# Kernel optimization log

Hardware: AMD Instinct MI355X
Metric: run time of the kernel (lower is better)

## Reference

```python
import jax, jax.numpy as jnp
import numpy as np

B, T, N, D, E = 16, 12, 512, 128, 32  # batch, time, nodes, model_dim, node_emb_dim


def setup_inputs() -> dict:
    key = jax.random.key(0)
    ks = jax.random.split(key, 7)
    return {
        "value": jax.random.normal(ks[0], (B, T, N, D), dtype=jnp.float32),
        "emb": jax.random.normal(ks[1], (T, N, E), dtype=jnp.float32),
        "attn_mask": jax.random.randint(ks[2], (B, N, N), 0, 2, dtype=jnp.int32),
        "W_qk": jax.random.normal(ks[3], (E, D), dtype=jnp.float32) * (1.0 / np.sqrt(E)),
        "b_qk": jax.random.normal(ks[4], (D,), dtype=jnp.float32) * 0.02,
        "W_v": jax.random.normal(ks[5], (D, D), dtype=jnp.float32) * (1.0 / np.sqrt(D)),
        "b_v": jax.random.normal(ks[6], (D,), dtype=jnp.float32) * 0.02,
    }


def reference(value, emb, attn_mask, W_qk, b_qk, W_v, b_v):
    # qk projection shared between query and key: [T, N, D]
    qk = emb @ W_qk + b_qk
    # query: softmax over feature dim D
    q = jax.nn.softmax(qk, axis=-1)                      # [T, N, D]
    # key: transpose then softmax over node dim N
    k = jax.nn.softmax(jnp.swapaxes(qk, -1, -2), axis=-1)  # [T, D, N]
    # value projection (note: out_proj in __init__ is unused in forward)
    v = value @ W_v + b_v                                # [B, T, N, D]
    # batch-independent base attention score, then broadcast over batch
    score = jnp.einsum('tnd,tdm->tnm', q, k)             # [T, N, N]
    score = jnp.broadcast_to(score[None], (value.shape[0],) + score.shape)  # [B, T, N, N]
    # masked fill: mask [B, N, N] -> [B, 1, N, N]
    score = jnp.where(attn_mask[:, None] == 0, jnp.float32(-1e9), score)
    out = jnp.einsum('btnm,btmd->btnd', score, v)         # [B, T, N, D]
    return out
```

## Files before the change

kernel.cpp:

```cpp
#include <hip/hip_runtime.h>

#define B_ 16
#define T_ 12
#define N_ 512
#define D_ 128
#define E_ 32

typedef __attribute__((ext_vector_type(8))) unsigned short u16x8;
typedef __attribute__((ext_vector_type(8))) __bf16 bf16x8;
typedef __attribute__((ext_vector_type(4))) float f32x4;

static __device__ __forceinline__ unsigned short f2bf(float f) {
    unsigned u = __float_as_uint(f);
    unsigned r = (u + 0x7fffu + ((u >> 16) & 1u)) >> 16;
    return (unsigned short)r;
}

__global__ __launch_bounds__(256) void kP1(const float* __restrict__ emb,
                                           const float* __restrict__ Wqk,
                                           const float* __restrict__ bqk,
                                           float* __restrict__ qk,
                                           unsigned short* __restrict__ qb,
                                           const int* __restrict__ mask,
                                           unsigned* __restrict__ mb,
                                           const float* __restrict__ Wv,
                                           unsigned short* __restrict__ WvT) {
    int bid = blockIdx.x;
    int tid = threadIdx.x;
    if (bid >= 2048) {
        int i = (bid - 2048) * 256 + tid;
        int d = i >> 7, k = i & 127;
        WvT[d * 128 + k] = f2bf(Wv[k * 128 + d]);
        return;
    }
    if (bid >= 1536) {
        int o = (bid - 1536) * 256 + tid;
        const int* mp = mask + (size_t)o * 32;
        unsigned bits = 0;
#pragma unroll
        for (int j = 0; j < 32; j += 4) {
            int4 m4 = *(const int4*)&mp[j];
            bits |= (m4.x ? 1u : 0u) << j;
            bits |= (m4.y ? 1u : 0u) << (j + 1);
            bits |= (m4.z ? 1u : 0u) << (j + 2);
            bits |= (m4.w ? 1u : 0u) << (j + 3);
        }
        mb[o] = bits;
        return;
    }
    int wave = tid >> 6, lane = tid & 63;
    int tn = bid * 4 + wave;
    const float* er = emb + (size_t)tn * E_;
    float a0 = bqk[lane], a1 = bqk[lane + 64];
#pragma unroll
    for (int e = 0; e < E_; ++e) {
        float ev = er[e];
        a0 = fmaf(ev, Wqk[e * D_ + lane], a0);
        a1 = fmaf(ev, Wqk[e * D_ + lane + 64], a1);
    }
    float* qr = qk + (size_t)tn * D_;
    qr[lane] = a0;
    qr[lane + 64] = a1;
    float mx = fmaxf(a0, a1);
#pragma unroll
    for (int s = 32; s > 0; s >>= 1) mx = fmaxf(mx, __shfl_xor(mx, s, 64));
    float e0 = __expf(a0 - mx), e1 = __expf(a1 - mx);
    float sum = e0 + e1;
#pragma unroll
    for (int s = 32; s > 0; s >>= 1) sum += __shfl_xor(sum, s, 64);
    float inv = 1.f / sum;
    unsigned short* qo = qb + (size_t)tn * D_;
    qo[lane] = f2bf(e0 * inv);
    qo[lane + 64] = f2bf(e1 * inv);
}

__global__ __launch_bounds__(256) void kA2n(const float* __restrict__ qk,
                                            unsigned short* __restrict__ kN) {
    int t = blockIdx.x >> 5;
    int d0 = (blockIdx.x & 31) * 4;
    int tid = threadIdx.x;
    int dc = tid & 3, ni = tid >> 2;
    const float* base = qk + (size_t)t * N_ * D_ + d0 + dc;
    float vals[8];
    float mx = -1e30f;
#pragma unroll
    for (int j = 0; j < 8; ++j) {
        vals[j] = base[(size_t)(ni + 64 * j) * D_];
        mx = fmaxf(mx, vals[j]);
    }
    __shared__ float red[64][5];
    red[ni][dc] = mx;
    __syncthreads();
#pragma unroll
    for (int s = 32; s > 0; s >>= 1) {
        if (ni < s) red[ni][dc] = fmaxf(red[ni][dc], red[ni + s][dc]);
        __syncthreads();
    }
    mx = red[0][dc];
    float sum = 0.f;
#pragma unroll
    for (int j = 0; j < 8; ++j) {
        vals[j] = __expf(vals[j] - mx);
        sum += vals[j];
    }
    __syncthreads();
    red[ni][dc] = sum;
    __syncthreads();
#pragma unroll
    for (int s = 32; s > 0; s >>= 1) {
        if (ni < s) red[ni][dc] += red[ni + s][dc];
        __syncthreads();
    }
    float inv = 1.f / red[0][dc];
    unsigned short* op = kN + (size_t)t * N_ * D_ + d0 + dc;
#pragma unroll
    for (int j = 0; j < 8; ++j)
        op[(size_t)(ni + 64 * j) * D_] = f2bf(vals[j] * inv);
}

__global__ __launch_bounds__(256) void kF(const unsigned short* __restrict__ qb,
                                          const unsigned short* __restrict__ kN,
                                          unsigned short* __restrict__ sc,
                                          const float* __restrict__ value,
                                          const unsigned short* __restrict__ WvT,
                                          const float* __restrict__ bv,
                                          unsigned short* __restrict__ vT) {
    __shared__ unsigned short shl[2][128 * 72];
    int bid = blockIdx.x;
    int tid = threadIdx.x;

    int wave = tid >> 6, lane = tid & 63;
    int q = lane >> 4, lr = lane & 15;
    int rbase = (wave & 1) * 64, cbase = (wave >> 1) * 64;

    f32x4 acc[4][4];
#pragma unroll
    for (int i = 0; i < 4; ++i)
#pragma unroll
        for (int j = 0; j < 4; ++j) acc[i][j] = (f32x4){0.f, 0.f, 0.f, 0.f};

    if (bid < 192) {
        int mt = bid & 3, nt = (bid >> 2) & 3, t = bid >> 4;
        int n0 = nt * 128, m0 = mt * 128;
        unsigned short* Qs = shl[0];
        unsigned short* Ks = shl[1];
        const unsigned short* qp = qb + (size_t)t * N_ * D_ + (size_t)n0 * D_;
        const unsigned short* kp = kN + (size_t)t * N_ * D_ + (size_t)m0 * D_;

        for (int c = 0; c < 2; ++c) {
            int k0 = c * 64;
            __syncthreads();
#pragma unroll
            for (int i = 0; i < 4; ++i) {
                int lin = tid + i * 256;
                int r = lin >> 3, seg = lin & 7;
                *(u16x8*)&Qs[r * 72 + seg * 8] =
                    *(const u16x8*)&qp[(size_t)r * D_ + k0 + seg * 8];
                *(u16x8*)&Ks[r * 72 + seg * 8] =
                    *(const u16x8*)&kp[(size_t)r * D_ + k0 + seg * 8];
            }
            __syncthreads();
#pragma unroll
            for (int kk = 0; kk < 2; ++kk) {
                bf16x8 a[4], b[4];
#pragma unroll
                for (int i = 0; i < 4; ++i)
                    a[i] = *(const bf16x8*)&Qs[(rbase + 16 * i + lr) * 72 + kk * 32 + q * 8];
#pragma unroll
                for (int j = 0; j < 4; ++j)
                    b[j] = *(const bf16x8*)&Ks[(cbase + 16 * j + lr) * 72 + kk * 32 + q * 8];
#pragma unroll
                for (int i = 0; i < 4; ++i)
#pragma unroll
                    for (int j = 0; j < 4; ++j)
                        acc[i][j] = __builtin_amdgcn_mfma_f32_16x16x32_bf16(
                            a[i], b[j], acc[i][j], 0, 0, 0);
            }
        }
        unsigned short* sp = sc + (size_t)t * N_ * N_;
#pragma unroll
        for (int i = 0; i < 4; ++i)
#pragma unroll
            for (int j = 0; j < 4; ++j) {
                int row0 = n0 + rbase + 16 * i + q * 4;
                int col = m0 + cbase + 16 * j + lr;
#pragma unroll
                for (int e = 0; e < 4; ++e)
                    sp[(size_t)(row0 + e) * N_ + col] = f2bf(acc[i][j][e]);
            }
        return;
    }

    {
        int idx = bid - 192;
        int mt = idx & 3, bt = idx >> 2;
        int m0 = mt * 128;
        unsigned short* Ws = shl[0];
        unsigned short* Vs = shl[1];
        const float* vp = value + ((size_t)bt * N_ + m0) * D_;

        for (int c = 0; c < 2; ++c) {
            int k0 = c * 64;
            __syncthreads();
#pragma unroll
            for (int i = 0; i < 4; ++i) {
                int lin = tid + i * 256;
                int r = lin >> 3, seg = lin & 7;
                *(u16x8*)&Ws[r * 72 + seg * 8] =
                    *(const u16x8*)&WvT[r * 128 + k0 + seg * 8];
            }
#pragma unroll
            for (int i = 0; i < 8; ++i) {
                int lin = tid + i * 256;
                int r = lin >> 4, c4 = lin & 15;
                float4 f = *(const float4*)&vp[(size_t)r * D_ + k0 + c4 * 4];
                ushort4 o;
                o.x = f2bf(f.x); o.y = f2bf(f.y); o.z = f2bf(f.z); o.w = f2bf(f.w);
                *(ushort4*)&Vs[r * 72 + c4 * 4] = o;
            }
            __syncthreads();
#pragma unroll
            for (int kk = 0; kk < 2; ++kk) {
                bf16x8 a[4], b[4];
#pragma unroll
                for (int i = 0; i < 4; ++i)
                    a[i] = *(const bf16x8*)&Ws[(rbase + 16 * i + lr) * 72 + kk * 32 + q * 8];
#pragma unroll
                for (int j = 0; j < 4; ++j)
                    b[j] = *(const bf16x8*)&Vs[(cbase + 16 * j + lr) * 72 + kk * 32 + q * 8];
#pragma unroll
                for (int i = 0; i < 4; ++i)
#pragma unroll
                    for (int j = 0; j < 4; ++j)
                        acc[i][j] = __builtin_amdgcn_mfma_f32_16x16x32_bf16(
                            a[i], b[j], acc[i][j], 0, 0, 0);
            }
        }
        unsigned short* op = vT + (size_t)bt * N_ * D_;
#pragma unroll
        for (int i = 0; i < 4; ++i) {
            int row0 = rbase + 16 * i + q * 4;
#pragma unroll
            for (int j = 0; j < 4; ++j) {
                int col = m0 + cbase + 16 * j + lr;
#pragma unroll
                for (int e = 0; e < 4; ++e)
                    op[(size_t)(row0 + e) * N_ + col] = f2bf(acc[i][j][e] + bv[row0 + e]);
            }
        }
    }
}

__global__ __launch_bounds__(256) void kC(const unsigned short* __restrict__ sc,
                                          const unsigned* __restrict__ mb,
                                          const unsigned short* __restrict__ vT,
                                          float* __restrict__ out) {
    int n0 = blockIdx.x * 128;
    int t = blockIdx.y, b = blockIdx.z;
    int tid = threadIdx.x;
    int wave = tid >> 6, lane = tid & 63;
    int q = lane >> 4, lr = lane & 15;
    int rbase = (wave & 1) * 64, cbase = (wave >> 1) * 64;

    __shared__ unsigned short Ss[128 * 72];
    __shared__ unsigned short Vs[128 * 72];

    const unsigned short* scp = sc + (size_t)t * N_ * N_ + (size_t)n0 * N_;
    const unsigned short* vtp = vT + ((size_t)(b * T_ + t)) * N_ * D_;
    const unsigned* mbp = mb + ((size_t)b * N_ + n0) * 16;

    const unsigned short NEG = 0xCE6E;

    f32x4 acc[4][4];
#pragma unroll
    for (int i = 0; i < 4; ++i)
#pragma unroll
        for (int j = 0; j < 4; ++j) acc[i][j] = (f32x4){0.f, 0.f, 0.f, 0.f};

    int sr = tid >> 1, sh2 = tid & 1;
    const unsigned short* sg = scp + (size_t)sr * N_ + sh2 * 32;
    const unsigned short* vg = vtp + (size_t)sr * N_ + sh2 * 32;
    const unsigned* mwp = mbp + sr * 16 + sh2;

    u16x8 sreg[4], vreg[4];
    unsigned mw;
#pragma unroll
    for (int p = 0; p < 4; ++p) {
        sreg[p] = *(const u16x8*)(sg + p * 8);
        vreg[p] = *(const u16x8*)(vg + p * 8);
    }
    mw = mwp[0];

    for (int kc = 0; kc < 8; ++kc) {
        if (kc) __syncthreads();
        unsigned short* Sd = &Ss[sr * 72 + sh2 * 32];
        unsigned short* Vd = &Vs[sr * 72 + sh2 * 32];
#pragma unroll
        for (int p = 0; p < 4; ++p) {
            unsigned bits = mw >> (p * 8);
            u16x8 o;
#pragma unroll
            for (int j = 0; j < 8; ++j)
                o[j] = ((bits >> j) & 1u) ? sreg[p][j] : NEG;
            *(u16x8*)(Sd + p * 8) = o;
            *(u16x8*)(Vd + p * 8) = vreg[p];
        }
        __syncthreads();
        if (kc < 7) {
            int off = (kc + 1) * 64;
#pragma unroll
            for (int p = 0; p < 4; ++p) {
                sreg[p] = *(const u16x8*)(sg + off + p * 8);
                vreg[p] = *(const u16x8*)(vg + off + p * 8);
            }
            mw = mwp[(kc + 1) * 2];
        }
#pragma unroll
        for (int ks = 0; ks < 2; ++ks) {
            bf16x8 a[4], bfr[4];
#pragma unroll
            for (int i = 0; i < 4; ++i)
                a[i] = *(const bf16x8*)&Ss[(rbase + 16 * i + lr) * 72 + ks * 32 + q * 8];
#pragma unroll
            for (int j = 0; j < 4; ++j)
                bfr[j] = *(const bf16x8*)&Vs[(cbase + 16 * j + lr) * 72 + ks * 32 + q * 8];
#pragma unroll
            for (int i = 0; i < 4; ++i)
#pragma unroll
                for (int j = 0; j < 4; ++j)
                    acc[i][j] = __builtin_amdgcn_mfma_f32_16x16x32_bf16(
                        a[i], bfr[j], acc[i][j], 0, 0, 0);
        }
    }

    float* ob = out + ((size_t)(b * T_ + t)) * N_ * D_;
#pragma unroll
    for (int i = 0; i < 4; ++i) {
#pragma unroll
        for (int j = 0; j < 4; ++j) {
            int row0 = n0 + rbase + 16 * i + q * 4;
            int col = cbase + 16 * j + lr;
#pragma unroll
            for (int e = 0; e < 4; ++e)
                ob[(size_t)(row0 + e) * D_ + col] = acc[i][j][e];
        }
    }
}

extern "C" void kernel_launch(void* const* d_in, const int* in_sizes, int n_in,
                              void* d_out, int out_size, void* d_ws, size_t ws_size,
                              hipStream_t stream) {
    const float* value = (const float*)d_in[0];
    const float* emb   = (const float*)d_in[1];
    const int*   mask  = (const int*)d_in[2];
    const float* Wqk   = (const float*)d_in[3];
    const float* bqk   = (const float*)d_in[4];
    const float* Wv    = (const float*)d_in[5];
    const float* bvv   = (const float*)d_in[6];
    float* out = (float*)d_out;

    float* ws = (float*)d_ws;
    float*          qkf  = ws;
    unsigned short* qb   = (unsigned short*)(ws + 786432);
    unsigned short* kNb  = (unsigned short*)(ws + 1179648);
    unsigned short* scb  = (unsigned short*)(ws + 1572864);
    unsigned short* vtb  = (unsigned short*)(ws + 3145728);
    unsigned short* WvTb = (unsigned short*)(ws + 9437184);
    unsigned*       mbp  = (unsigned*)(ws + 9445376);

    kP1<<<2112, 256, 0, stream>>>(emb, Wqk, bqk, qkf, qb, mask, mbp, Wv, WvTb);
    kA2n<<<384, 256, 0, stream>>>(qkf, kNb);
    kF<<<960, 256, 0, stream>>>(qb, kNb, scb, value, WvTb, bvv, vtb);
    kC<<<dim3(4, T_, B_), 256, 0, stream>>>(scb, mbp, vtb, out);
}
```

Measured before the change: 170.3 us.

## Fuse key softmax into projection kernel and prefetch second K-chunk in GEMM tiles

```diff
diff --git a/kernel.cpp b/kernel.cpp
--- a/kernel.cpp
+++ b/kernel.cpp
@@ -19,22 +19,24 @@
 __global__ __launch_bounds__(256) void kP1(const float* __restrict__ emb,
                                            const float* __restrict__ Wqk,
                                            const float* __restrict__ bqk,
-                                           float* __restrict__ qk,
                                            unsigned short* __restrict__ qb,
+                                           unsigned short* __restrict__ kN,
                                            const int* __restrict__ mask,
                                            unsigned* __restrict__ mb,
                                            const float* __restrict__ Wv,
                                            unsigned short* __restrict__ WvT) {
+    __shared__ float red[64][5];
     int bid = blockIdx.x;
     int tid = threadIdx.x;
-    if (bid >= 2048) {
-        int i = (bid - 2048) * 256 + tid;
+
+    if (bid >= 2432) {
+        int i = (bid - 2432) * 256 + tid;
         int d = i >> 7, k = i & 127;
         WvT[d * 128 + k] = f2bf(Wv[k * 128 + d]);
         return;
     }
-    if (bid >= 1536) {
-        int o = (bid - 1536) * 256 + tid;
+    if (bid >= 1920) {
+        int o = (bid - 1920) * 256 + tid;
         const int* mp = mask + (size_t)o * 32;
         unsigned bits = 0;
 #pragma unroll
@@ -48,6 +50,63 @@
         mb[o] = bits;
         return;
     }
+    if (bid >= 1536) {
+        int idx = bid - 1536;
+        int t = idx >> 5;
+        int d0 = (idx & 31) * 4;
+        int dc = tid & 3, ni = tid >> 2;
+        int d = d0 + dc;
+        float wcol[E_];
+#pragma unroll
+        for (int e = 0; e < E_; ++e) wcol[e] = Wqk[e * D_ + d];
+        float bias = bqk[d];
+        float vals[8];
+        float mx = -1e30f;
+#pragma unroll
+        for (int j = 0; j < 8; ++j) {
+            int n = ni + 64 * j;
+            const float* er = emb + ((size_t)t * N_ + n) * E_;
+            float a = bias;
+#pragma unroll
+            for (int e = 0; e < E_; e += 4) {
+                float4 ev = *(const float4*)&er[e];
+                a = fmaf(ev.x, wcol[e], a);
+                a = fmaf(ev.y, wcol[e + 1], a);
+                a = fmaf(ev.z, wcol[e + 2], a);
+                a = fmaf(ev.w, wcol[e + 3], a);
+            }
+            vals[j] = a;
+            mx = fmaxf(mx, a);
+        }
+        red[ni][dc] = mx;
+        __syncthreads();
+#pragma unroll
+        for (int s = 32; s > 0; s >>= 1) {
+            if (ni < s) red[ni][dc] = fmaxf(red[ni][dc], red[ni + s][dc]);
+            __syncthreads();
+        }
+        mx = red[0][dc];
+        float sum = 0.f;
+#pragma unroll
+        for (int j = 0; j < 8; ++j) {
+            vals[j] = __expf(vals[j] - mx);
+            sum += vals[j];
+        }
+        __syncthreads();
+        red[ni][dc] = sum;
+        __syncthreads();
+#pragma unroll
+        for (int s = 32; s > 0; s >>= 1) {
+            if (ni < s) red[ni][dc] += red[ni + s][dc];
+            __syncthreads();
+        }
+        float inv = 1.f / red[0][dc];
+        unsigned short* op = kN + (size_t)t * N_ * D_ + d;
+#pragma unroll
+        for (int j = 0; j < 8; ++j)
+            op[(size_t)(ni + 64 * j) * D_] = f2bf(vals[j] * inv);
+        return;
+    }
     int wave = tid >> 6, lane = tid & 63;
     int tn = bid * 4 + wave;
     const float* er = emb + (size_t)tn * E_;
@@ -58,9 +117,6 @@
         a0 = fmaf(ev, Wqk[e * D_ + lane], a0);
         a1 = fmaf(ev, Wqk[e * D_ + lane + 64], a1);
     }
-    float* qr = qk + (size_t)tn * D_;
-    qr[lane] = a0;
-    qr[lane + 64] = a1;
     float mx = fmaxf(a0, a1);
 #pragma unroll
     for (int s = 32; s > 0; s >>= 1) mx = fmaxf(mx, __shfl_xor(mx, s, 64));
@@ -72,50 +128,6 @@
     unsigned short* qo = qb + (size_t)tn * D_;
     qo[lane] = f2bf(e0 * inv);
     qo[lane + 64] = f2bf(e1 * inv);
-}
-
-__global__ __launch_bounds__(256) void kA2n(const float* __restrict__ qk,
-                                            unsigned short* __restrict__ kN) {
-    int t = blockIdx.x >> 5;
-    int d0 = (blockIdx.x & 31) * 4;
-    int tid = threadIdx.x;
-    int dc = tid & 3, ni = tid >> 2;
-    const float* base = qk + (size_t)t * N_ * D_ + d0 + dc;
-    float vals[8];
-    float mx = -1e30f;
-#pragma unroll
-    for (int j = 0; j < 8; ++j) {
-        vals[j] = base[(size_t)(ni + 64 * j) * D_];
-        mx = fmaxf(mx, vals[j]);
-    }
-    __shared__ float red[64][5];
-    red[ni][dc] = mx;
-    __syncthreads();
-#pragma unroll
-    for (int s = 32; s > 0; s >>= 1) {
-        if (ni < s) red[ni][dc] = fmaxf(red[ni][dc], red[ni + s][dc]);
-        __syncthreads();
-    }
-    mx = red[0][dc];
-    float sum = 0.f;
-#pragma unroll
-    for (int j = 0; j < 8; ++j) {
-        vals[j] = __expf(vals[j] - mx);
-        sum += vals[j];
-    }
-    __syncthreads();
-    red[ni][dc] = sum;
-    __syncthreads();
-#pragma unroll
-    for (int s = 32; s > 0; s >>= 1) {
-        if (ni < s) red[ni][dc] += red[ni + s][dc];
-        __syncthreads();
-    }
-    float inv = 1.f / red[0][dc];
-    unsigned short* op = kN + (size_t)t * N_ * D_ + d0 + dc;
-#pragma unroll
-    for (int j = 0; j < 8; ++j)
-        op[(size_t)(ni + 64 * j) * D_] = f2bf(vals[j] * inv);
 }
 
 __global__ __launch_bounds__(256) void kF(const unsigned short* __restrict__ qb,
@@ -147,19 +159,26 @@
         const unsigned short* qp = qb + (size_t)t * N_ * D_ + (size_t)n0 * D_;
         const unsigned short* kp = kN + (size_t)t * N_ * D_ + (size_t)m0 * D_;
 
+        int r = tid >> 1, seg2 = (tid & 1) * 4;
+        u16x8 qr[4], kr[4];
+#pragma unroll
+        for (int i = 0; i < 4; ++i) {
+            qr[i] = *(const u16x8*)&qp[(size_t)r * D_ + (seg2 + i) * 8];
+            kr[i] = *(const u16x8*)&kp[(size_t)r * D_ + (seg2 + i) * 8];
+        }
+#pragma unroll
+        for (int i = 0; i < 4; ++i) {
+            *(u16x8*)&Qs[r * 72 + (seg2 + i) * 8] = qr[i];
+            *(u16x8*)&Ks[r * 72 + (seg2 + i) * 8] = kr[i];
+        }
+        __syncthreads();
+#pragma unroll
+        for (int i = 0; i < 4; ++i) {
+            qr[i] = *(const u16x8*)&qp[(size_t)r * D_ + 64 + (seg2 + i) * 8];
+            kr[i] = *(const u16x8*)&kp[(size_t)r * D_ + 64 + (seg2 + i) * 8];
+        }
+#pragma unroll
         for (int c = 0; c < 2; ++c) {
-            int k0 = c * 64;
-            __syncthreads();
-#pragma unroll
-            for (int i = 0; i < 4; ++i) {
-                int lin = tid + i * 256;
-                int r = lin >> 3, seg = lin & 7;
-                *(u16x8*)&Qs[r * 72 + seg * 8] =
-                    *(const u16x8*)&qp[(size_t)r * D_ + k0 + seg * 8];
-                *(u16x8*)&Ks[r * 72 + seg * 8] =
-                    *(const u16x8*)&kp[(size_t)r * D_ + k0 + seg * 8];
-            }
-            __syncthreads();
 #pragma unroll
             for (int kk = 0; kk < 2; ++kk) {
                 bf16x8 a[4], b[4];
@@ -175,6 +194,15 @@
                     for (int j = 0; j < 4; ++j)
                         acc[i][j] = __builtin_amdgcn_mfma_f32_16x16x32_bf16(
                             a[i], b[j], acc[i][j], 0, 0, 0);
+            }
+            if (c == 0) {
+                __syncthreads();
+#pragma unroll
+                for (int i = 0; i < 4; ++i) {
+                    *(u16x8*)&Qs[r * 72 + (seg2 + i) * 8] = qr[i];
+                    *(u16x8*)&Ks[r * 72 + (seg2 + i) * 8] = kr[i];
+                }
+                __syncthreads();
             }
         }
         unsigned short* sp = sc + (size_t)t * N_ * N_;
@@ -199,26 +227,42 @@
         unsigned short* Vs = shl[1];
         const float* vp = value + ((size_t)bt * N_ + m0) * D_;
 
+        int r = tid >> 1, seg2 = (tid & 1) * 4;
+        u16x8 wr[4];
+        float4 vr[8];
+#pragma unroll
+        for (int i = 0; i < 4; ++i)
+            wr[i] = *(const u16x8*)&WvT[r * 128 + (seg2 + i) * 8];
+#pragma unroll
+        for (int i = 0; i < 8; ++i) {
+            int lin = tid + i * 256;
+            int vrr = lin >> 4, c4 = lin & 15;
+            vr[i] = *(const float4*)&vp[(size_t)vrr * D_ + c4 * 4];
+        }
+#pragma unroll
+        for (int i = 0; i < 4; ++i)
+            *(u16x8*)&Ws[r * 72 + (seg2 + i) * 8] = wr[i];
+#pragma unroll
+        for (int i = 0; i < 8; ++i) {
+            int lin = tid + i * 256;
+            int vrr = lin >> 4, c4 = lin & 15;
+            ushort4 o;
+            o.x = f2bf(vr[i].x); o.y = f2bf(vr[i].y);
+            o.z = f2bf(vr[i].z); o.w = f2bf(vr[i].w);
+            *(ushort4*)&Vs[vrr * 72 + c4 * 4] = o;
+        }
+        __syncthreads();
+#pragma unroll
+        for (int i = 0; i < 4; ++i)
+            wr[i] = *(const u16x8*)&WvT[r * 128 + 64 + (seg2 + i) * 8];
+#pragma unroll
+        for (int i = 0; i < 8; ++i) {
+            int lin = tid + i * 256;
+            int vrr = lin >> 4, c4 = lin & 15;
+            vr[i] = *(const float4*)&vp[(size_t)vrr * D_ + 64 + c4 * 4];
+        }
+#pragma unroll
         for (int c = 0; c < 2; ++c) {
-            int k0 = c * 64;
-            __syncthreads();
-#pragma unroll
-            for (int i = 0; i < 4; ++i) {
-                int lin = tid + i * 256;
-                int r = lin >> 3, seg = lin & 7;
-                *(u16x8*)&Ws[r * 72 + seg * 8] =
-                    *(const u16x8*)&WvT[r * 128 + k0 + seg * 8];
-            }
-#pragma unroll
-            for (int i = 0; i < 8; ++i) {
-                int lin = tid + i * 256;
-                int r = lin >> 4, c4 = lin & 15;
-                float4 f = *(const float4*)&vp[(size_t)r * D_ + k0 + c4 * 4];
-                ushort4 o;
-                o.x = f2bf(f.x); o.y = f2bf(f.y); o.z = f2bf(f.z); o.w = f2bf(f.w);
-                *(ushort4*)&Vs[r * 72 + c4 * 4] = o;
-            }
-            __syncthreads();
 #pragma unroll
             for (int kk = 0; kk < 2; ++kk) {
                 bf16x8 a[4], b[4];
@@ -234,6 +278,22 @@
                     for (int j = 0; j < 4; ++j)
                         acc[i][j] = __builtin_amdgcn_mfma_f32_16x16x32_bf16(
                             a[i], b[j], acc[i][j], 0, 0, 0);
+            }
+            if (c == 0) {
+                __syncthreads();
+#pragma unroll
+                for (int i = 0; i < 4; ++i)
+                    *(u16x8*)&Ws[r * 72 + (seg2 + i) * 8] = wr[i];
+#pragma unroll
+                for (int i = 0; i < 8; ++i) {
+                    int lin = tid + i * 256;
+                    int vrr = lin >> 4, c4 = lin & 15;
+                    ushort4 o;
+                    o.x = f2bf(vr[i].x); o.y = f2bf(vr[i].y);
+                    o.z = f2bf(vr[i].z); o.w = f2bf(vr[i].w);
+                    *(ushort4*)&Vs[vrr * 72 + c4 * 4] = o;
+                }
+                __syncthreads();
             }
         }
         unsigned short* op = vT + (size_t)bt * N_ * D_;
@@ -360,16 +420,14 @@
     float* out = (float*)d_out;
 
     float* ws = (float*)d_ws;
-    float*          qkf  = ws;
-    unsigned short* qb   = (unsigned short*)(ws + 786432);
-    unsigned short* kNb  = (unsigned short*)(ws + 1179648);
-    unsigned short* scb  = (unsigned short*)(ws + 1572864);
-    unsigned short* vtb  = (unsigned short*)(ws + 3145728);
-    unsigned short* WvTb = (unsigned short*)(ws + 9437184);
-    unsigned*       mbp  = (unsigned*)(ws + 9445376);
-
-    kP1<<<2112, 256, 0, stream>>>(emb, Wqk, bqk, qkf, qb, mask, mbp, Wv, WvTb);
-    kA2n<<<384, 256, 0, stream>>>(qkf, kNb);
+    unsigned short* qb   = (unsigned short*)(ws);
+    unsigned short* kNb  = (unsigned short*)(ws + 393216);
+    unsigned short* scb  = (unsigned short*)(ws + 786432);
+    unsigned short* vtb  = (unsigned short*)(ws + 2359296);
+    unsigned short* WvTb = (unsigned short*)(ws + 8650752);
+    unsigned*       mbp  = (unsigned*)(ws + 8658944);
+
+    kP1<<<2496, 256, 0, stream>>>(emb, Wqk, bqk, qb, kNb, mask, mbp, Wv, WvTb);
     kF<<<960, 256, 0, stream>>>(qb, kNb, scb, value, WvTb, bvv, vtb);
     kC<<<dim3(4, T_, B_), 256, 0, stream>>>(scb, mbp, vtb, out);
 }
```

New measurement: 171.5 us. About the same (+0.7%).
